# Kernel tuning notes

Hardware: AMD Instinct MI355X
Metric: run time of the kernel (lower is better)

## Reference

```python
import jax, jax.numpy as jnp
import numpy as np

DIM = 1024
NHEAD = 16
HEAD_DIM = DIM // NHEAD
EPS = 1e-5


def setup_inputs() -> dict:
    key = jax.random.key(0)
    ks = jax.random.split(key, 10)
    s = 1.0 / np.sqrt(DIM)
    x = jax.random.normal(ks[0], (4, 2048, DIM), dtype=jnp.float32)
    Wq = jax.random.uniform(ks[1], (DIM, DIM), minval=-s, maxval=s, dtype=jnp.float32)
    bq = jax.random.uniform(ks[2], (DIM,), minval=-s, maxval=s, dtype=jnp.float32)
    Wk = jax.random.uniform(ks[3], (DIM, DIM), minval=-s, maxval=s, dtype=jnp.float32)
    bk = jax.random.uniform(ks[4], (DIM,), minval=-s, maxval=s, dtype=jnp.float32)
    Wv = jax.random.uniform(ks[5], (DIM, DIM), minval=-s, maxval=s, dtype=jnp.float32)
    bv = jax.random.uniform(ks[6], (DIM,), minval=-s, maxval=s, dtype=jnp.float32)
    Wo = jax.random.uniform(ks[7], (DIM, DIM), minval=-s, maxval=s, dtype=jnp.float32)
    bo = jax.random.uniform(ks[8], (DIM,), minval=-s, maxval=s, dtype=jnp.float32)
    gamma = jnp.ones((DIM,), dtype=jnp.float32)
    beta = jnp.zeros((DIM,), dtype=jnp.float32)
    return {"x": x, "Wq": Wq, "bq": bq, "Wk": Wk, "bk": bk, "Wv": Wv,
            "bv": bv, "Wo": Wo, "bo": bo, "gamma": gamma, "beta": beta}


def reference(x, Wq, bq, Wk, bk, Wv, bv, Wo, bo, gamma, beta):
    B, S, D = x.shape
    H, Dh = NHEAD, HEAD_DIM

    def heads(t):  # [B,S,D] -> [B,H,S,Dh]
        return t.reshape(B, S, H, Dh).transpose(0, 2, 1, 3)

    Q = heads(x @ Wq.T + bq)
    K = heads(x @ Wk.T + bk)
    V = heads(x @ Wv.T + bv)

    scores = jnp.einsum('bhqd,bhkd->bhqk', Q, K) / np.sqrt(Dh).astype(np.float32)
    causal = jnp.tril(jnp.ones((S, S), dtype=bool))
    scores = jnp.where(causal, scores, -jnp.inf)
    attn = jax.nn.softmax(scores, axis=-1)
    ctx = jnp.einsum('bhqk,bhkd->bhqd', attn, V)  # [B,H,S,Dh]
    ctx = ctx.transpose(0, 2, 1, 3).reshape(B, S, D)

    out = ctx @ Wo.T + bo
    out = out + x
    mu = jnp.mean(out, axis=-1, keepdims=True)
    var = jnp.mean(jnp.square(out - mu), axis=-1, keepdims=True)
    out = (out - mu) / jnp.sqrt(var + EPS) * gamma + beta
    return out
```

## Files before the change

### kernel.cpp

```cpp
#include <hip/hip_runtime.h>
#include <hip/hip_bf16.h>
#include <stdint.h>

#define DIM 1024
#define SEQ 2048
#define TOK 8192

typedef __hip_bfloat16 bf16;
using bf16x8 = __attribute__((ext_vector_type(8))) short;
using bf16x4 = __attribute__((ext_vector_type(4))) short;
using f32x4  = __attribute__((ext_vector_type(4))) float;

struct __align__(8) bh4 { bf16 a, b, c, d; };

__device__ __forceinline__ void g2lds16(const void* g, void* l) {
    __builtin_amdgcn_global_load_lds(
        (const __attribute__((address_space(1))) void*)g,
        (__attribute__((address_space(3))) void*)l,
        16, 0, 0);
}

__device__ __forceinline__ float hexp2(float x) {
    float r;
    asm("v_exp_f32 %0, %1" : "=v"(r) : "v"(x));
    return r;
}
__device__ __forceinline__ unsigned cvtpk(float lo, float hi) {
    unsigned r;
    asm("v_cvt_pk_bf16_f32 %0, %1, %2" : "=v"(r) : "v"(lo), "v"(hi));
    return r;
}
__device__ __forceinline__ float hrcp(float x) {
    float r;
    asm("v_rcp_f32 %0, %1" : "=v"(r) : "v"(x));
    return r;
}

__device__ __forceinline__ short bfb(float f) {
    __hip_bfloat16 h = __float2bfloat16(f);
    return *reinterpret_cast<short*>(&h);
}

__global__ __launch_bounds__(256) void cast_all_kernel(
    const float* __restrict__ x,  const float* __restrict__ wq,
    const float* __restrict__ wk, const float* __restrict__ wv,
    const float* __restrict__ wo, bf16* __restrict__ xb, bf16* __restrict__ wb)
{
    const long idx = (long)blockIdx.x * 256 + threadIdx.x;
    const long e = idx * 4;
    const float* src;
    bf16* dst;
    if (e < 8388608L) { src = x + e; dst = xb + e; }
    else {
        const long j = e - 8388608L;
        const int  w = (int)(j >> 20);
        const long off = j & 1048575L;
        src = ((w == 0) ? wq : (w == 1) ? wk : (w == 2) ? wv : wo) + off;
        dst = wb + ((long)w << 20) + off;
    }
    const float4 v = *(const float4*)src;
    bh4 o;
    o.a = __float2bfloat16(v.x); o.b = __float2bfloat16(v.y);
    o.c = __float2bfloat16(v.z); o.d = __float2bfloat16(v.w);
    *(bh4*)dst = o;
}

template<int MODE>
__global__ __launch_bounds__(256) void gemm_bt_kernel(
    const bf16* __restrict__ A, const bf16* __restrict__ B,
    const float* __restrict__ bias0, const float* __restrict__ bias1,
    const float* __restrict__ bias2,
    bf16* __restrict__ outQ, bf16* __restrict__ outK, bf16* __restrict__ outVt)
{
    __shared__ __align__(16) bf16 As[128 * 64];
    __shared__ __align__(16) bf16 Bs[128 * 64];
    const int tid  = threadIdx.x;
    const int wave = tid >> 6;
    const int lane = tid & 63;
    const int bm = blockIdx.x;
    const int bn = blockIdx.y;
    const int wm = (wave >> 1) * 64;
    const int wn = (wave & 1) * 64;
    const int lcol = lane & 15;
    const int lrow = lane >> 4;
    const int l8 = lane >> 3, l7 = lane & 7;
    const int swz = (l7 ^ l8) * 8;

    f32x4 acc[4][4] = {};

    const bf16* Ab = A + ((long)bm * 128 + wave * 32 + l8) * 1024 + swz;
    const bf16* Bb = B + ((long)bn * 128 + wave * 32 + l8) * 1024 + swz;
    char* AsW = (char*)As + (wave * 32) * 128;
    char* BsW = (char*)Bs + (wave * 32) * 128;

    #pragma unroll
    for (int i = 0; i < 4; ++i) {
        g2lds16(Ab + (long)i * 8 * 1024, AsW + i * 1024);
        g2lds16(Bb + (long)i * 8 * 1024, BsW + i * 1024);
    }
    for (int kt = 0; kt < 1024; kt += 64) {
        __syncthreads();
        bf16x8 af[4][2], bfr[4][2];
        #pragma unroll
        for (int m = 0; m < 4; ++m) {
            const int row = wm + m * 16 + lcol;
            #pragma unroll
            for (int kk = 0; kk < 2; ++kk) {
                const int off = (row * 128 + kk * 64 + lrow * 16) ^ ((row & 7) << 4);
                af[m][kk] = *(const bf16x8*)((const char*)As + off);
            }
        }
        #pragma unroll
        for (int n = 0; n < 4; ++n) {
            const int row = wn + n * 16 + lcol;
            #pragma unroll
            for (int kk = 0; kk < 2; ++kk) {
                const int off = (row * 128 + kk * 64 + lrow * 16) ^ ((row & 7) << 4);
                bfr[n][kk] = *(const bf16x8*)((const char*)Bs + off);
            }
        }
        __syncthreads();
        if (kt + 64 < 1024) {
            #pragma unroll
            for (int i = 0; i < 4; ++i) {
                g2lds16(Ab + (long)i * 8 * 1024 + kt + 64, AsW + i * 1024);
                g2lds16(Bb + (long)i * 8 * 1024 + kt + 64, BsW + i * 1024);
            }
        }
        #pragma unroll
        for (int kk = 0; kk < 2; ++kk)
            #pragma unroll
            for (int m = 0; m < 4; ++m)
                #pragma unroll
                for (int n = 0; n < 4; ++n)
                    acc[m][n] = __builtin_amdgcn_mfma_f32_16x16x32_bf16(
                        af[m][kk], bfr[n][kk], acc[m][n], 0, 0, 0);
    }

    const int rbase = lrow * 4;
    if (MODE == 0) {
        const int which = bn >> 3;
        const float* bias = (which == 0) ? bias0 : (which == 1) ? bias1 : bias2;
        const float QSCALE = 0.125f * 1.44269504089f;
        #pragma unroll
        for (int m = 0; m < 4; ++m) {
            const long gr = (long)bm * 128 + wm + m * 16 + rbase;
            #pragma unroll
            for (int n = 0; n < 4; ++n) {
                const int gc = bn * 128 + wn + n * 16 + lcol;
                const int nn = gc & 1023;
                const float bv_ = bias[nn];
                #pragma unroll
                for (int r = 0; r < 4; ++r) {
                    const long t = gr + r;
                    const float v = acc[m][n][r] + bv_;
                    if (which == 0)      outQ[t * 1024 + nn] = __float2bfloat16(v * QSCALE);
                    else if (which == 1) outK[t * 1024 + nn] = __float2bfloat16(v);
                    else {
                        const long bb = t >> 11;
                        const long s  = t & 2047;
                        const int  hh = nn >> 6, dh = nn & 63;
                        outVt[((bb * 16 + hh) * 64 + dh) * 2048 + s] = __float2bfloat16(v);
                    }
                }
            }
        }
    } else {
        #pragma unroll
        for (int m = 0; m < 4; ++m) {
            const long gr = (long)bm * 128 + wm + m * 16 + rbase;
            #pragma unroll
            for (int n = 0; n < 4; ++n) {
                const int gc = bn * 128 + wn + n * 16 + lcol;
                const float bv_ = bias0[gc];
                #pragma unroll
                for (int r = 0; r < 4; ++r) {
                    const long t = gr + r;
                    outQ[t * 1024 + gc] = __float2bfloat16(acc[m][n][r] + bv_);
                }
            }
        }
    }
}

__global__ __launch_bounds__(256) void attn_kernel(
    const bf16* __restrict__ Qb, const bf16* __restrict__ Kb,
    const bf16* __restrict__ Vt, bf16* __restrict__ ctx)
{
    __shared__ __align__(16) bf16 Ks[2][2][4096];
    __shared__ __align__(16) bf16 Vs[2][2][4096];
    const int tid = threadIdx.x, wv = tid >> 6, lane = tid & 63;
    const int id  = blockIdx.y * 16 + blockIdx.x;
    const int lid = (id & 7) * 128 + (id >> 3);
    const int bh  = lid >> 4;
    const int pr  = lid & 15;
    const int b = bh >> 4, h = bh & 15;
    const bf16* Qh = Qb + (long)b * SEQ * DIM + h * 64;
    const bf16* Kh = Kb + (long)b * SEQ * DIM + h * 64;
    const bf16* Vh = Vt + (long)bh * 64 * SEQ;
    const int lcol = lane & 15;
    const int lrow = lane >> 4;
    const int l8 = lane >> 3, l7 = lane & 7;
    const int swz = (l7 ^ l8) * 8;
    const int kprow = (wv >> 1) * 32 + (l8 >> 2) * 8 + (wv & 1) * 4 + (l8 & 3);
    const bf16* kSrc = Kh + (long)kprow * DIM + swz;
    const bf16* vSrc = Vh + (long)(wv * 16 + l8) * SEQ + swz;

    const bf16x8 ONES = { (short)0x3F80, (short)0x3F80, (short)0x3F80, (short)0x3F80,
                          (short)0x3F80, (short)0x3F80, (short)0x3F80, (short)0x3F80 };

    #pragma unroll
    for (int half = 0; half < 2; ++half) {
        const int qt = half ? (31 - pr) : pr;
        const int qtb = qt * 64;
        const int q0 = qtb + wv * 16;
        bf16x8 qf[2];
        #pragma unroll
        for (int kk = 0; kk < 2; ++kk)
            qf[kk] = *(const bf16x8*)&Qh[(long)(q0 + lcol) * DIM + kk * 32 + lrow * 8];

        f32x4 o_acc[4] = {};
        f32x4 l_acc = {};
        const int itn = (qt >> 1) + 1;
        #pragma unroll
        for (int sub = 0; sub < 2; ++sub) {
            char* dK = (char*)Ks[0][sub] + wv * 2048;
            char* dV = (char*)Vs[0][sub] + wv * 2048;
            #pragma unroll
            for (int i = 0; i < 2; ++i) {
                g2lds16(kSrc + (long)(sub * 64 + i * 16) * DIM, dK + i * 1024);
                g2lds16(vSrc + sub * 64 + (long)i * 8 * SEQ, dV + i * 1024);
            }
        }
        __syncthreads();
        for (int it = 0; it < itn; ++it) {
            if (it + 1 < itn) {
                const long ko = (long)(it + 1) * 128;
                #pragma unroll
                for (int sub = 0; sub < 2; ++sub) {
                    const bf16* kS = kSrc + (ko + sub * 64) * DIM;
                    const bf16* vS = vSrc + ko + sub * 64;
                    char* dK = (char*)Ks[(it + 1) & 1][sub] + wv * 2048;
                    char* dV = (char*)Vs[(it + 1) & 1][sub] + wv * 2048;
                    #pragma unroll
                    for (int i = 0; i < 2; ++i) {
                        g2lds16(kS + (long)i * 16 * DIM, dK + i * 1024);
                        g2lds16(vS + (long)i * 8 * SEQ, dV + i * 1024);
                    }
                }
            }
            #pragma unroll
            for (int sub = 0; sub < 2; ++sub) {
                const int kbase = it * 128 + sub * 64;
                if (kbase > qtb) continue;
                const char* Kp = (const char*)Ks[it & 1][sub];
                const char* Vp = (const char*)Vs[it & 1][sub];
                f32x4 s_acc[4] = {};
                __builtin_amdgcn_s_setprio(1);
                #pragma unroll
                for (int n = 0; n < 4; ++n) {
                    const int krow = n * 16 + lcol;
                    #pragma unroll
                    for (int kk = 0; kk < 2; ++kk) {
                        const int off = (krow * 128 + kk * 64 + lrow * 16) ^ ((krow & 7) << 4);
                        bf16x8 kf = *(const bf16x8*)(Kp + off);
                        s_acc[n] = __builtin_amdgcn_mfma_f32_16x16x32_bf16(kf, qf[kk], s_acc[n], 0, 0, 0);
                    }
                }
                __builtin_amdgcn_s_setprio(0);
                if (kbase == qtb) {
                    const int qg = q0 + lcol;
                    #pragma unroll
                    for (int n = 0; n < 4; ++n)
                        #pragma unroll
                        for (int r = 0; r < 4; ++r) {
                            const int ka = kbase + ((n >> 1) << 5) + lrow * 8 + ((n & 1) << 2) + r;
                            if (ka > qg) s_acc[n][r] = -1e30f;
                        }
                }
                #pragma unroll
                for (int n = 0; n < 4; ++n)
                    #pragma unroll
                    for (int r = 0; r < 4; ++r)
                        s_acc[n][r] = hexp2(s_acc[n][r]);
                union { unsigned u[4]; bf16x8 v; } pkA, pkB;
                pkA.u[0] = cvtpk(s_acc[0][0], s_acc[0][1]);
                pkA.u[1] = cvtpk(s_acc[0][2], s_acc[0][3]);
                pkA.u[2] = cvtpk(s_acc[1][0], s_acc[1][1]);
                pkA.u[3] = cvtpk(s_acc[1][2], s_acc[1][3]);
                pkB.u[0] = cvtpk(s_acc[2][0], s_acc[2][1]);
                pkB.u[1] = cvtpk(s_acc[2][2], s_acc[2][3]);
                pkB.u[2] = cvtpk(s_acc[3][0], s_acc[3][1]);
                pkB.u[3] = cvtpk(s_acc[3][2], s_acc[3][3]);
                const bf16x8 paA = pkA.v, paB = pkB.v;
                __builtin_amdgcn_s_setprio(1);
                l_acc = __builtin_amdgcn_mfma_f32_16x16x32_bf16(paA, ONES, l_acc, 0, 0, 0);
                l_acc = __builtin_amdgcn_mfma_f32_16x16x32_bf16(paB, ONES, l_acc, 0, 0, 0);
                #pragma unroll
                for (int d = 0; d < 4; ++d) {
                    const int vrow = d * 16 + lcol;
                    const int offA = (vrow * 128 + lrow * 16) ^ ((vrow & 7) << 4);
                    const int offB = offA ^ 64;
                    bf16x8 vfA = *(const bf16x8*)(Vp + offA);
                    o_acc[d] = __builtin_amdgcn_mfma_f32_16x16x32_bf16(paA, vfA, o_acc[d], 0, 0, 0);
                    bf16x8 vfB = *(const bf16x8*)(Vp + offB);
                    o_acc[d] = __builtin_amdgcn_mfma_f32_16x16x32_bf16(paB, vfB, o_acc[d], 0, 0, 0);
                }
                __builtin_amdgcn_s_setprio(0);
            }
            __syncthreads();
        }
        float rl[4];
        #pragma unroll
        for (int r = 0; r < 4; ++r) rl[r] = hrcp(l_acc[r]);
        #pragma unroll
        for (int d = 0; d < 4; ++d)
            #pragma unroll
            for (int r = 0; r < 4; ++r) {
                const float v = o_acc[d][r] * rl[r];
                ctx[(long)(b * SEQ + q0 + lrow * 4 + r) * DIM + h * 64 + d * 16 + lcol] = __float2bfloat16(v);
            }
    }
}

__global__ __launch_bounds__(256) void ln_kernel(
    const bf16* __restrict__ proj, const float* __restrict__ x,
    float* __restrict__ out,
    const float* __restrict__ gamma, const float* __restrict__ beta)
{
    const long row = blockIdx.x;
    const int tid = threadIdx.x;
    const int c = tid * 4;
    const bh4  pv = *(const bh4*)&proj[row * 1024 + c];
    const float4 xv = *(const float4*)&x[row * 1024 + c];
    float4 v;
    v.x = xv.x + __bfloat162float(pv.a);
    v.y = xv.y + __bfloat162float(pv.b);
    v.z = xv.z + __bfloat162float(pv.c);
    v.w = xv.w + __bfloat162float(pv.d);
    float s  = v.x + v.y + v.z + v.w;
    float s2 = v.x * v.x + v.y * v.y + v.z * v.z + v.w * v.w;
    #pragma unroll
    for (int off = 1; off < 64; off <<= 1) {
        s  += __shfl_xor(s, off);
        s2 += __shfl_xor(s2, off);
    }
    __shared__ float red[8];
    if ((tid & 63) == 0) { red[tid >> 6] = s; red[4 + (tid >> 6)] = s2; }
    __syncthreads();
    s  = red[0] + red[1] + red[2] + red[3];
    s2 = red[4] + red[5] + red[6] + red[7];
    const float mu = s * (1.0f / 1024.0f);
    const float var = fmaxf(s2 * (1.0f / 1024.0f) - mu * mu, 0.0f);
    const float rstd = rsqrtf(var + 1e-5f);
    const float4 g  = *(const float4*)&gamma[c];
    const float4 bb = *(const float4*)&beta[c];
    float4 o;
    o.x = (v.x - mu) * rstd * g.x + bb.x;
    o.y = (v.y - mu) * rstd * g.y + bb.y;
    o.z = (v.z - mu) * rstd * g.z + bb.z;
    o.w = (v.w - mu) * rstd * g.w + bb.w;
    *(float4*)&out[row * 1024 + c] = o;
}

extern "C" void kernel_launch(void* const* d_in, const int* in_sizes, int n_in,
                              void* d_out, int out_size, void* d_ws, size_t ws_size,
                              hipStream_t stream)
{
    const float* x     = (const float*)d_in[0];
    const float* Wq    = (const float*)d_in[1];
    const float* bq    = (const float*)d_in[2];
    const float* Wk    = (const float*)d_in[3];
    const float* bk    = (const float*)d_in[4];
    const float* Wv    = (const float*)d_in[5];
    const float* bv    = (const float*)d_in[6];
    const float* Wo    = (const float*)d_in[7];
    const float* bo    = (const float*)d_in[8];
    const float* gamma = (const float*)d_in[9];
    const float* beta  = (const float*)d_in[10];
    float* out = (float*)d_out;

    char* ws = (char*)d_ws;
    bf16* xb  = (bf16*)(ws);
    bf16* wb  = (bf16*)(ws + (16L << 20));
    bf16* Qb  = (bf16*)(ws + (24L << 20));
    bf16* Kb  = (bf16*)(ws + (40L << 20));
    bf16* Vt  = (bf16*)(ws + (56L << 20));
    bf16* ctx = (bf16*)(ws + (72L << 20));
    bf16* proj = Qb;

    cast_all_kernel<<<12288, 256, 0, stream>>>(x, Wq, Wk, Wv, Wo, xb, wb);
    gemm_bt_kernel<0><<<dim3(64, 24), 256, 0, stream>>>(
        xb, wb, bq, bk, bv, Qb, Kb, Vt);
    attn_kernel<<<dim3(16, 64), 256, 0, stream>>>(Qb, Kb, Vt, ctx);
    gemm_bt_kernel<1><<<dim3(64, 8), 256, 0, stream>>>(
        ctx, wb + 3L * 1048576, bo, nullptr, nullptr, proj, nullptr, nullptr);
    ln_kernel<<<8192, 256, 0, stream>>>(proj, x, out, gamma, beta);
}
```

Baseline: 191.3 us.

## Double attention query tile to 128 rows per block for K/V reuse

Each attention block now handles 128 query rows instead of 64, with every wave computing two 16-row query groups that share each K and V fragment loaded from LDS. This halves the grid and the number of times each K/V tile is streamed from global memory into LDS, and amortises LDS reads over twice the MFMA work. In exchange it uses more registers per wave, launches only 512 blocks, and masks more wasted work on diagonal tiles, which could lower occupancy or worsen load balance.

```diff
diff --git a/kernel.cpp b/kernel.cpp
--- a/kernel.cpp
+++ b/kernel.cpp
@@ -190,10 +190,10 @@
     __shared__ __align__(16) bf16 Ks[2][2][4096];
     __shared__ __align__(16) bf16 Vs[2][2][4096];
     const int tid = threadIdx.x, wv = tid >> 6, lane = tid & 63;
-    const int id  = blockIdx.y * 16 + blockIdx.x;
-    const int lid = (id & 7) * 128 + (id >> 3);
-    const int bh  = lid >> 4;
-    const int pr  = lid & 15;
+    const int id  = blockIdx.y * 8 + blockIdx.x;
+    const int lid = (id & 7) * 64 + (id >> 3);
+    const int bh  = lid >> 3;
+    const int pr  = lid & 7;
     const int b = bh >> 4, h = bh & 15;
     const bf16* Qh = Qb + (long)b * SEQ * DIM + h * 64;
     const bf16* Kh = Kb + (long)b * SEQ * DIM + h * 64;
@@ -211,17 +211,19 @@
 
     #pragma unroll
     for (int half = 0; half < 2; ++half) {
-        const int qt = half ? (31 - pr) : pr;
-        const int qtb = qt * 64;
-        const int q0 = qtb + wv * 16;
-        bf16x8 qf[2];
-        #pragma unroll
-        for (int kk = 0; kk < 2; ++kk)
-            qf[kk] = *(const bf16x8*)&Qh[(long)(q0 + lcol) * DIM + kk * 32 + lrow * 8];
-
-        f32x4 o_acc[4] = {};
-        f32x4 l_acc = {};
-        const int itn = (qt >> 1) + 1;
+        const int qt = half ? (15 - pr) : pr;
+        const int qtb = qt * 128;
+        const int q0 = qtb + wv * 32;
+        bf16x8 qf[2][2];
+        #pragma unroll
+        for (int g = 0; g < 2; ++g)
+            #pragma unroll
+            for (int kk = 0; kk < 2; ++kk)
+                qf[g][kk] = *(const bf16x8*)&Qh[(long)(q0 + g * 16 + lcol) * DIM + kk * 32 + lrow * 8];
+
+        f32x4 o_acc[2][4] = {};
+        f32x4 l_acc[2] = {};
+        const int itn = qt + 1;
         #pragma unroll
         for (int sub = 0; sub < 2; ++sub) {
             char* dK = (char*)Ks[0][sub] + wv * 2048;
@@ -252,10 +254,10 @@
             #pragma unroll
             for (int sub = 0; sub < 2; ++sub) {
                 const int kbase = it * 128 + sub * 64;
-                if (kbase > qtb) continue;
+                if (kbase > qtb + 64) continue;
                 const char* Kp = (const char*)Ks[it & 1][sub];
                 const char* Vp = (const char*)Vs[it & 1][sub];
-                f32x4 s_acc[4] = {};
+                f32x4 s_acc[2][4] = {};
                 __builtin_amdgcn_s_setprio(1);
                 #pragma unroll
                 for (int n = 0; n < 4; ++n) {
@@ -264,62 +266,72 @@
                     for (int kk = 0; kk < 2; ++kk) {
                         const int off = (krow * 128 + kk * 64 + lrow * 16) ^ ((krow & 7) << 4);
                         bf16x8 kf = *(const bf16x8*)(Kp + off);
-                        s_acc[n] = __builtin_amdgcn_mfma_f32_16x16x32_bf16(kf, qf[kk], s_acc[n], 0, 0, 0);
+                        s_acc[0][n] = __builtin_amdgcn_mfma_f32_16x16x32_bf16(kf, qf[0][kk], s_acc[0][n], 0, 0, 0);
+                        s_acc[1][n] = __builtin_amdgcn_mfma_f32_16x16x32_bf16(kf, qf[1][kk], s_acc[1][n], 0, 0, 0);
                     }
                 }
                 __builtin_amdgcn_s_setprio(0);
-                if (kbase == qtb) {
-                    const int qg = q0 + lcol;
+                if (kbase + 64 > qtb) {
+                    #pragma unroll
+                    for (int g = 0; g < 2; ++g) {
+                        const int qg = q0 + g * 16 + lcol;
+                        #pragma unroll
+                        for (int n = 0; n < 4; ++n)
+                            #pragma unroll
+                            for (int r = 0; r < 4; ++r) {
+                                const int ka = kbase + ((n >> 1) << 5) + lrow * 8 + ((n & 1) << 2) + r;
+                                if (ka > qg) s_acc[g][n][r] = -1e30f;
+                            }
+                    }
+                }
+                __builtin_amdgcn_s_setprio(1);
+                #pragma unroll
+                for (int g = 0; g < 2; ++g) {
                     #pragma unroll
                     for (int n = 0; n < 4; ++n)
                         #pragma unroll
-                        for (int r = 0; r < 4; ++r) {
-                            const int ka = kbase + ((n >> 1) << 5) + lrow * 8 + ((n & 1) << 2) + r;
-                            if (ka > qg) s_acc[n][r] = -1e30f;
-                        }
-                }
-                #pragma unroll
-                for (int n = 0; n < 4; ++n)
+                        for (int r = 0; r < 4; ++r)
+                            s_acc[g][n][r] = hexp2(s_acc[g][n][r]);
+                    union { unsigned u[4]; bf16x8 v; } pkA, pkB;
+                    pkA.u[0] = cvtpk(s_acc[g][0][0], s_acc[g][0][1]);
+                    pkA.u[1] = cvtpk(s_acc[g][0][2], s_acc[g][0][3]);
+                    pkA.u[2] = cvtpk(s_acc[g][1][0], s_acc[g][1][1]);
+                    pkA.u[3] = cvtpk(s_acc[g][1][2], s_acc[g][1][3]);
+                    pkB.u[0] = cvtpk(s_acc[g][2][0], s_acc[g][2][1]);
+                    pkB.u[1] = cvtpk(s_acc[g][2][2], s_acc[g][2][3]);
+                    pkB.u[2] = cvtpk(s_acc[g][3][0], s_acc[g][3][1]);
+                    pkB.u[3] = cvtpk(s_acc[g][3][2], s_acc[g][3][3]);
+                    const bf16x8 paA = pkA.v, paB = pkB.v;
+                    l_acc[g] = __builtin_amdgcn_mfma_f32_16x16x32_bf16(paA, ONES, l_acc[g], 0, 0, 0);
+                    l_acc[g] = __builtin_amdgcn_mfma_f32_16x16x32_bf16(paB, ONES, l_acc[g], 0, 0, 0);
                     #pragma unroll
-                    for (int r = 0; r < 4; ++r)
-                        s_acc[n][r] = hexp2(s_acc[n][r]);
-                union { unsigned u[4]; bf16x8 v; } pkA, pkB;
-                pkA.u[0] = cvtpk(s_acc[0][0], s_acc[0][1]);
-                pkA.u[1] = cvtpk(s_acc[0][2], s_acc[0][3]);
-                pkA.u[2] = cvtpk(s_acc[1][0], s_acc[1][1]);
-                pkA.u[3] = cvtpk(s_acc[1][2], s_acc[1][3]);
-                pkB.u[0] = cvtpk(s_acc[2][0], s_acc[2][1]);
-                pkB.u[1] = cvtpk(s_acc[2][2], s_acc[2][3]);
-                pkB.u[2] = cvtpk(s_acc[3][0], s_acc[3][1]);
-                pkB.u[3] = cvtpk(s_acc[3][2], s_acc[3][3]);
-                const bf16x8 paA = pkA.v, paB = pkB.v;
-                __builtin_amdgcn_s_setprio(1);
-                l_acc = __builtin_amdgcn_mfma_f32_16x16x32_bf16(paA, ONES, l_acc, 0, 0, 0);
-                l_acc = __builtin_amdgcn_mfma_f32_16x16x32_bf16(paB, ONES, l_acc, 0, 0, 0);
-                #pragma unroll
-                for (int d = 0; d < 4; ++d) {
-                    const int vrow = d * 16 + lcol;
-                    const int offA = (vrow * 128 + lrow * 16) ^ ((vrow & 7) << 4);
-                    const int offB = offA ^ 64;
-                    bf16x8 vfA = *(const bf16x8*)(Vp + offA);
-                    o_acc[d] = __builtin_amdgcn_mfma_f32_16x16x32_bf16(paA, vfA, o_acc[d], 0, 0, 0);
-                    bf16x8 vfB = *(const bf16x8*)(Vp + offB);
-                    o_acc[d] = __builtin_amdgcn_mfma_f32_16x16x32_bf16(paB, vfB, o_acc[d], 0, 0, 0);
+                    for (int d = 0; d < 4; ++d) {
+                        const int vrow = d * 16 + lcol;
+                        const int offA = (vrow * 128 + lrow * 16) ^ ((vrow & 7) << 4);
+                        const int offB = offA ^ 64;
+                        bf16x8 vfA = *(const bf16x8*)(Vp + offA);
+                        o_acc[g][d] = __builtin_amdgcn_mfma_f32_16x16x32_bf16(paA, vfA, o_acc[g][d], 0, 0, 0);
+                        bf16x8 vfB = *(const bf16x8*)(Vp + offB);
+                        o_acc[g][d] = __builtin_amdgcn_mfma_f32_16x16x32_bf16(paB, vfB, o_acc[g][d], 0, 0, 0);
+                    }
                 }
                 __builtin_amdgcn_s_setprio(0);
             }
             __syncthreads();
         }
-        float rl[4];
-        #pragma unroll
-        for (int r = 0; r < 4; ++r) rl[r] = hrcp(l_acc[r]);
-        #pragma unroll
-        for (int d = 0; d < 4; ++d)
-            #pragma unroll
-            for (int r = 0; r < 4; ++r) {
-                const float v = o_acc[d][r] * rl[r];
-                ctx[(long)(b * SEQ + q0 + lrow * 4 + r) * DIM + h * 64 + d * 16 + lcol] = __float2bfloat16(v);
-            }
+        #pragma unroll
+        for (int g = 0; g < 2; ++g) {
+            float rl[4];
+            #pragma unroll
+            for (int r = 0; r < 4; ++r) rl[r] = hrcp(l_acc[g][r]);
+            #pragma unroll
+            for (int d = 0; d < 4; ++d)
+                #pragma unroll
+                for (int r = 0; r < 4; ++r) {
+                    const float v = o_acc[g][d][r] * rl[r];
+                    ctx[(long)(b * SEQ + q0 + g * 16 + lrow * 4 + r) * DIM + h * 64 + d * 16 + lcol] = __float2bfloat16(v);
+                }
+        }
     }
 }
 
@@ -392,7 +404,7 @@
     cast_all_kernel<<<12288, 256, 0, stream>>>(x, Wq, Wk, Wv, Wo, xb, wb);
     gemm_bt_kernel<0><<<dim3(64, 24), 256, 0, stream>>>(
         xb, wb, bq, bk, bv, Qb, Kb, Vt);
-    attn_kernel<<<dim3(16, 64), 256, 0, stream>>>(Qb, Kb, Vt, ctx);
+    attn_kernel<<<dim3(8, 64), 256, 0, stream>>>(Qb, Kb, Vt, ctx);
     gemm_bt_kernel<1><<<dim3(64, 8), 256, 0, stream>>>(
         ctx, wb + 3L * 1048576, bo, nullptr, nullptr, proj, nullptr, nullptr);
     ln_kernel<<<8192, 256, 0, stream>>>(proj, x, out, gamma, beta);
```

After: 173.9 us. -9.1%, faster.
